# Optimization experiments

Hardware: AMD Instinct MI355X
Metric: run time of the kernel (lower is better)

The kernel has to match this reference:

```python
import jax, jax.numpy as jnp
import numpy as np

B, N, D, H = 8, 384, 256, 1024

def setup_inputs() -> dict:
    key = jax.random.key(0)
    ks = jax.random.split(key, 8)
    x = jax.random.normal(ks[0], (B, N, D), jnp.float32)
    adj = jnp.ones((B, N, N), jnp.float32)
    box_num = jax.random.randint(ks[1], (B, 1), 1, N + 1).astype(jnp.int64)
    box_num = box_num.at[0, 0].set(N)  # original code assumes max(box_num) == N
    fc1_w = jax.random.normal(ks[2], (H, D), jnp.float32) * (1.0 / np.sqrt(D))
    fc1_b = jnp.zeros((H,), jnp.float32)
    fc2_w = jax.random.normal(ks[3], (D, H), jnp.float32) * (1.0 / np.sqrt(H))
    fc2_b = jnp.zeros((D,), jnp.float32)
    learn_w = jax.random.uniform(ks[4], (D,), jnp.float32)  # uniform_(0,1) init
    return {"x": x, "adj": adj, "box_num": box_num,
            "fc1_w": fc1_w, "fc1_b": fc1_b, "fc2_w": fc2_w, "fc2_b": fc2_b,
            "learn_w": learn_w}

def reference(x, adj, box_num, fc1_w, fc1_b, fc2_w, fc2_b, learn_w):
    # mlp: fc2(relu(fc1(x)))  -> x_hat (B,N,D)
    x_hat = jnp.maximum(x @ fc1_w.T + fc1_b, 0.0) @ fc2_w.T + fc2_b
    # dynamic mask: -1 where either node i or j is padding, 0 otherwise
    valid = jnp.arange(N)[None, :] < box_num            # (B,N)
    pair_valid = valid[:, None, :] & valid[:, :, None]  # (B,N,N)
    mask = jnp.where(pair_valid, 0.0, -1.0)             # (B,N,N)
    # pairwise weighted L1 distance: einsum('bijd,d->bij', |x_i - x_j| + mask, w)
    # mask broadcasts over d, so its contribution is mask * sum(w) (same math,
    # avoids a second (B,N,N,D) materialization)
    absdiff = jnp.abs(x_hat[:, :, None, :] - x_hat[:, None, :, :])  # (B,N,N,D)
    dist = jnp.einsum('bijd,d->bij', absdiff, learn_w) + mask * jnp.sum(learn_w)
    out = jax.nn.leaky_relu(dist, negative_slope=0.01)
    out = out - jnp.max(out, axis=-1, keepdims=True)
    soft_adj = adj * jnp.exp(out)
    soft_adj = soft_adj / jnp.sum(soft_adj, axis=-1, keepdims=True) + 1e-10
    return soft_adj, x_hat
```

## Files before the change

### kernel.cpp

```cpp
#include <hip/hip_runtime.h>
#include <math.h>

#define B_ 8
#define N_ 384
#define D_ 256
#define H_ 1024

typedef __bf16 bh;
typedef __bf16 bf16x8 __attribute__((ext_vector_type(8)));
typedef __bf16 bf16x4 __attribute__((ext_vector_type(4)));
typedef float  f32x4  __attribute__((ext_vector_type(4)));
typedef _Float16 h2 __attribute__((ext_vector_type(2)));

#define LDB 72

#if __has_builtin(__builtin_amdgcn_fdot2)
#define FDOT2(a,b,c) __builtin_amdgcn_fdot2((a),(b),(c),false)
#else
#define FDOT2(a,b,c) ((c) + (float)(a).x*(float)(b).x + (float)(a).y*(float)(b).y)
#endif

__device__ inline h2 habs2(h2 x) {
    unsigned u = __builtin_bit_cast(unsigned, x) & 0x7fff7fffu;
    return __builtin_bit_cast(h2, u);
}

__device__ inline void split2(float v, bh& h, bh& l) {
    h = (bh)v;
    l = (bh)(v - (float)h);
}

__device__ inline int load_boxnum(const int* __restrict__ p, int b) {
    bool is64 = ((p[1] | p[3] | p[5] | p[7]) == 0);
    return is64 ? p[2 * b] : p[b];
}

__global__ __launch_bounds__(256) void split3_kernel(
        const float* __restrict__ s0, bh* __restrict__ h0, bh* __restrict__ l0, int n0,
        const float* __restrict__ s1, bh* __restrict__ h1, bh* __restrict__ l1, int n1,
        const float* __restrict__ s2, bh* __restrict__ h2_, bh* __restrict__ l2, int n2)
{
    const int total = n0 + n1 + n2;
    for (int qd = blockIdx.x * blockDim.x + threadIdx.x; qd < total; qd += gridDim.x * blockDim.x) {
        const float* s; bh* ph; bh* pl; int i;
        if (qd < n0)           { s = s0; ph = h0;  pl = l0; i = qd; }
        else if (qd < n0 + n1) { s = s1; ph = h1;  pl = l1; i = qd - n0; }
        else                   { s = s2; ph = h2_; pl = l2; i = qd - n0 - n1; }
        float4 v = *(const float4*)(s + 4 * (size_t)i);
        bf16x4 hv, lv; bh hh, ll;
        split2(v.x, hh, ll); hv[0] = hh; lv[0] = ll;
        split2(v.y, hh, ll); hv[1] = hh; lv[1] = ll;
        split2(v.z, hh, ll); hv[2] = hh; lv[2] = ll;
        split2(v.w, hh, ll); hv[3] = hh; lv[3] = ll;
        *(bf16x4*)(ph + 4 * (size_t)i) = hv;
        *(bf16x4*)(pl + 4 * (size_t)i) = lv;
    }
}

__global__ __launch_bounds__(256) void gemm1_kernel(
        const bh* __restrict__ Ah_, const bh* __restrict__ Al_,
        const bh* __restrict__ Wh_, const bh* __restrict__ Wl_,
        const float* __restrict__ bias,
        bh* __restrict__ Ch, bh* __restrict__ Cl)
{
    __shared__ __align__(16) bh AhS[64 * LDB], AlS[64 * LDB], WhS[64 * LDB], WlS[64 * LDB];
    const int tid = threadIdx.x;
    const int m0 = blockIdx.y * 64, n0 = blockIdx.x * 64;
    const int r = tid >> 2, kq = (tid & 3) * 16;
    const int lane = tid & 63, wv_ = tid >> 6;
    const int wm = (wv_ & 1) * 32, wn = (wv_ >> 1) * 32;
    const int l15 = lane & 15, q = lane >> 4;

    f32x4 acc[2][2] = {};
    for (int k0 = 0; k0 < D_; k0 += 64) {
        const bh* pah = Ah_ + (size_t)(m0 + r) * D_ + k0 + kq;
        const bh* pal = Al_ + (size_t)(m0 + r) * D_ + k0 + kq;
        const bh* pwh = Wh_ + (size_t)(n0 + r) * D_ + k0 + kq;
        const bh* pwl = Wl_ + (size_t)(n0 + r) * D_ + k0 + kq;
        bf16x8 ah0 = *(const bf16x8*)pah, ah1 = *(const bf16x8*)(pah + 8);
        bf16x8 al0 = *(const bf16x8*)pal, al1 = *(const bf16x8*)(pal + 8);
        bf16x8 wh0 = *(const bf16x8*)pwh, wh1 = *(const bf16x8*)(pwh + 8);
        bf16x8 wl0 = *(const bf16x8*)pwl, wl1 = *(const bf16x8*)(pwl + 8);
        __syncthreads();
        *(bf16x8*)&AhS[r * LDB + kq] = ah0;  *(bf16x8*)&AhS[r * LDB + kq + 8] = ah1;
        *(bf16x8*)&AlS[r * LDB + kq] = al0;  *(bf16x8*)&AlS[r * LDB + kq + 8] = al1;
        *(bf16x8*)&WhS[r * LDB + kq] = wh0;  *(bf16x8*)&WhS[r * LDB + kq + 8] = wh1;
        *(bf16x8*)&WlS[r * LDB + kq] = wl0;  *(bf16x8*)&WlS[r * LDB + kq + 8] = wl1;
        __syncthreads();
        #pragma unroll
        for (int ks = 0; ks < 2; ks++) {
            const int kb = ks * 32 + q * 8;
            bf16x8 fah[2], fal[2], fwh[2], fwl[2];
            #pragma unroll
            for (int mi = 0; mi < 2; mi++) {
                int row = wm + mi * 16 + l15;
                fah[mi] = *(const bf16x8*)&AhS[row * LDB + kb];
                fal[mi] = *(const bf16x8*)&AlS[row * LDB + kb];
            }
            #pragma unroll
            for (int ni = 0; ni < 2; ni++) {
                int row = wn + ni * 16 + l15;
                fwh[ni] = *(const bf16x8*)&WhS[row * LDB + kb];
                fwl[ni] = *(const bf16x8*)&WlS[row * LDB + kb];
            }
            #pragma unroll
            for (int mi = 0; mi < 2; mi++)
                #pragma unroll
                for (int ni = 0; ni < 2; ni++) {
                    acc[mi][ni] = __builtin_amdgcn_mfma_f32_16x16x32_bf16(fah[mi], fwh[ni], acc[mi][ni], 0, 0, 0);
                    acc[mi][ni] = __builtin_amdgcn_mfma_f32_16x16x32_bf16(fah[mi], fwl[ni], acc[mi][ni], 0, 0, 0);
                    acc[mi][ni] = __builtin_amdgcn_mfma_f32_16x16x32_bf16(fal[mi], fwh[ni], acc[mi][ni], 0, 0, 0);
                }
        }
    }
    #pragma unroll
    for (int ni = 0; ni < 2; ni++) {
        int col = n0 + wn + ni * 16 + l15;
        float bb = bias[col];
        #pragma unroll
        for (int mi = 0; mi < 2; mi++)
            #pragma unroll
            for (int reg = 0; reg < 4; reg++) {
                int row = m0 + wm + mi * 16 + q * 4 + reg;
                float v = fmaxf(acc[mi][ni][reg] + bb, 0.f);
                bh h, l; split2(v, h, l);
                size_t off = (size_t)row * H_ + col;
                Ch[off] = h; Cl[off] = l;
            }
    }
}

__global__ __launch_bounds__(256) void gemm2_kernel(
        const bh* __restrict__ Ah_, const bh* __restrict__ Al_,
        const bh* __restrict__ Wh_, const bh* __restrict__ Wl_,
        const float* __restrict__ bias,
        float* __restrict__ C, _Float16* __restrict__ C16)
{
    __shared__ __align__(16) bh AhS[64 * LDB], AlS[64 * LDB], WhS[32 * LDB], WlS[32 * LDB];
    const int tid = threadIdx.x;
    const int m0 = blockIdx.y * 64, n0 = blockIdx.x * 32;
    const int lane = tid & 63, wv_ = tid >> 6;
    const int wm = wv_ * 16;
    const int l15 = lane & 15, q = lane >> 4;
    const int r = tid >> 2, kq = (tid & 3) * 16;
    const int rw = tid >> 3, kw = (tid & 7) * 8;

    f32x4 acc[2] = {};
    for (int k0 = 0; k0 < H_; k0 += 64) {
        const bh* pah = Ah_ + (size_t)(m0 + r) * H_ + k0 + kq;
        const bh* pal = Al_ + (size_t)(m0 + r) * H_ + k0 + kq;
        const bh* pwh = Wh_ + (size_t)(n0 + rw) * H_ + k0 + kw;
        const bh* pwl = Wl_ + (size_t)(n0 + rw) * H_ + k0 + kw;
        bf16x8 ah0 = *(const bf16x8*)pah, ah1 = *(const bf16x8*)(pah + 8);
        bf16x8 al0 = *(const bf16x8*)pal, al1 = *(const bf16x8*)(pal + 8);
        bf16x8 wh0 = *(const bf16x8*)pwh;
        bf16x8 wl0 = *(const bf16x8*)pwl;
        __syncthreads();
        *(bf16x8*)&AhS[r * LDB + kq] = ah0;  *(bf16x8*)&AhS[r * LDB + kq + 8] = ah1;
        *(bf16x8*)&AlS[r * LDB + kq] = al0;  *(bf16x8*)&AlS[r * LDB + kq + 8] = al1;
        *(bf16x8*)&WhS[rw * LDB + kw] = wh0;
        *(bf16x8*)&WlS[rw * LDB + kw] = wl0;
        __syncthreads();
        #pragma unroll
        for (int ks = 0; ks < 2; ks++) {
            const int kb = ks * 32 + q * 8;
            const int arow = wm + l15;
            bf16x8 fah = *(const bf16x8*)&AhS[arow * LDB + kb];
            bf16x8 fal = *(const bf16x8*)&AlS[arow * LDB + kb];
            #pragma unroll
            for (int ni = 0; ni < 2; ni++) {
                int row = ni * 16 + l15;
                bf16x8 fwh = *(const bf16x8*)&WhS[row * LDB + kb];
                bf16x8 fwl = *(const bf16x8*)&WlS[row * LDB + kb];
                acc[ni] = __builtin_amdgcn_mfma_f32_16x16x32_bf16(fah, fwh, acc[ni], 0, 0, 0);
                acc[ni] = __builtin_amdgcn_mfma_f32_16x16x32_bf16(fah, fwl, acc[ni], 0, 0, 0);
                acc[ni] = __builtin_amdgcn_mfma_f32_16x16x32_bf16(fal, fwh, acc[ni], 0, 0, 0);
            }
        }
    }
    #pragma unroll
    for (int ni = 0; ni < 2; ni++) {
        int col = n0 + ni * 16 + l15;
        float bb = bias[col];
        #pragma unroll
        for (int reg = 0; reg < 4; reg++) {
            int row = m0 + wm + q * 4 + reg;
            float v = acc[ni][reg] + bb;
            C[(size_t)row * D_ + col] = v;
            C16[(size_t)row * D_ + col] = (_Float16)v;
        }
    }
}

#define DLX 132
__global__ __launch_bounds__(512) void dist_kernel(const _Float16* __restrict__ xh16,
                                                   const float* __restrict__ w,
                                                   const int* __restrict__ box_num,
                                                   float* __restrict__ dist) {
    __shared__ __align__(16) unsigned X[128 * DLX];
    __shared__ unsigned WkS[128];
    const int bidx = blockIdx.x;
    const int b = bidx / 21;
    int p = bidx % 21;
    int ti = 0;
    while (p >= 6 - ti) { p -= 6 - ti; ti++; }
    const int tj = ti + p;
    const int i0 = ti * 64, j0 = tj * 64;
    const int tid = threadIdx.x;
    const int lane = tid & 63;

    float sumw = w[lane] + w[lane + 64] + w[lane + 128] + w[lane + 192];
    #pragma unroll
    for (int off = 32; off > 0; off >>= 1) sumw += __shfl_xor(sumw, off);

    if (tid < 128) {
        float2 wp = *(const float2*)&w[2 * tid];
        h2 wv = {(_Float16)wp.x, (_Float16)wp.y};
        WkS[tid] = __builtin_bit_cast(unsigned, wv);
    }

    const int sr = tid >> 2, koff = (tid & 3) * 64;
    const int grow = (sr < 64) ? (i0 + sr) : (j0 + sr - 64);
    const _Float16* src = xh16 + ((size_t)b * N_ + grow) * D_ + koff;
    #pragma unroll
    for (int ld = 0; ld < 8; ld++) {
        uint4 v = *(const uint4*)(src + ld * 8);
        int k2 = (koff >> 1) + ld * 4;
        X[(k2 + 0) * DLX + sr] = v.x;
        X[(k2 + 1) * DLX + sr] = v.y;
        X[(k2 + 2) * DLX + sr] = v.z;
        X[(k2 + 3) * DLX + sr] = v.w;
    }
    __syncthreads();

    const int tx = tid & 31, ty = tid >> 5;
    float acc[4][2] = {};
    #pragma unroll 4
    for (int k2 = 0; k2 < 128; k2++) {
        uint4 av = *(const uint4*)&X[k2 * DLX + ty * 4];
        uint2 bv = *(const uint2*)&X[k2 * DLX + 64 + tx * 2];
        h2 wv = __builtin_bit_cast(h2, WkS[k2]);
        h2 ai[4] = {__builtin_bit_cast(h2, av.x), __builtin_bit_cast(h2, av.y),
                    __builtin_bit_cast(h2, av.z), __builtin_bit_cast(h2, av.w)};
        h2 bj[2] = {__builtin_bit_cast(h2, bv.x), __builtin_bit_cast(h2, bv.y)};
        #pragma unroll
        for (int ii = 0; ii < 4; ii++)
            #pragma unroll
            for (int jj = 0; jj < 2; jj++) {
                h2 d = habs2(ai[ii] - bj[jj]);
                acc[ii][jj] = FDOT2(d, wv, acc[ii][jj]);
            }
    }

    const int bn = load_boxnum(box_num, b);
    float m[4][2];
    #pragma unroll
    for (int ii = 0; ii < 4; ii++) {
        int i = i0 + ty * 4 + ii;
        bool vi = i < bn;
        #pragma unroll
        for (int jj = 0; jj < 2; jj++) {
            int j = j0 + tx * 2 + jj;
            float v = acc[ii][jj];
            if (!(vi && (j < bn))) v -= sumw;
            m[ii][jj] = v > 0.f ? v : 0.01f * v;
        }
    }
    #pragma unroll
    for (int ii = 0; ii < 4; ii++) {
        int i = i0 + ty * 4 + ii;
        float2 o = {m[ii][0], m[ii][1]};
        *(float2*)&dist[((size_t)b * N_ + i) * N_ + j0 + tx * 2] = o;
    }
    #pragma unroll
    for (int jj = 0; jj < 2; jj++) {
        int j = j0 + tx * 2 + jj;
        float4 o = {m[0][jj], m[1][jj], m[2][jj], m[3][jj]};
        *(float4*)&dist[((size_t)b * N_ + j) * N_ + i0 + ty * 4] = o;
    }
}

__global__ __launch_bounds__(256) void softmax_kernel(float* __restrict__ sa,
                                                      const float* __restrict__ adj) {
    const int row = blockIdx.x * 4 + (threadIdx.x >> 6);
    const int t = threadIdx.x & 63;
    float* prow = sa + (size_t)row * N_;
    const float* arow = adj + (size_t)row * N_;
    float v[6];
    float m = -1e30f;
    #pragma unroll
    for (int qq = 0; qq < 6; qq++) { v[qq] = prow[t + qq * 64]; m = fmaxf(m, v[qq]); }
    #pragma unroll
    for (int off = 32; off > 0; off >>= 1) m = fmaxf(m, __shfl_xor(m, off));
    float e[6];
    float s = 0.f;
    #pragma unroll
    for (int qq = 0; qq < 6; qq++) { e[qq] = arow[t + qq * 64] * expf(v[qq] - m); s += e[qq]; }
    #pragma unroll
    for (int off = 32; off > 0; off >>= 1) s += __shfl_xor(s, off);
    float inv = 1.0f / s;
    #pragma unroll
    for (int qq = 0; qq < 6; qq++) prow[t + qq * 64] = e[qq] * inv + 1e-10f;
}

extern "C" void kernel_launch(void* const* d_in, const int* in_sizes, int n_in,
                              void* d_out, int out_size, void* d_ws, size_t ws_size,
                              hipStream_t stream) {
    const float* x       = (const float*)d_in[0];
    const float* adj     = (const float*)d_in[1];
    const int*   box_num = (const int*)d_in[2];
    const float* fc1_w   = (const float*)d_in[3];
    const float* fc1_b   = (const float*)d_in[4];
    const float* fc2_w   = (const float*)d_in[5];
    const float* fc2_b   = (const float*)d_in[6];
    const float* learn_w = (const float*)d_in[7];

    float* soft_adj = (float*)d_out;
    float* xhat     = (float*)d_out + (size_t)B_ * N_ * N_;

    const int BN = B_ * N_;

    bh* w1h = (bh*)d_ws;
    bh* w1l = w1h + (size_t)H_ * D_;
    bh* w2h = w1l + (size_t)H_ * D_;
    bh* w2l = w2h + (size_t)D_ * H_;
    _Float16* xh16 = (_Float16*)(w2l + (size_t)D_ * H_);
    bh* cbase = (bh*)(xh16 + (size_t)BN * D_);
    const size_t fixed_bytes = (size_t)4 * H_ * D_ * 2 + (size_t)BN * D_ * 2;
    const size_t per_row = (size_t)(D_ * 2 + H_ * 2) * 2;

    long long avail = (long long)ws_size - (long long)fixed_bytes;
    long long mr = (avail > 0) ? (avail / (long long)per_row) : 0;
    if (mr > BN) mr = BN;
    mr &= ~63LL;
    if (mr < 64) mr = 64;
    const int max_rows = (int)mr;

    bool first = true;
    for (int m0 = 0; m0 < BN; m0 += max_rows) {
        int rows = BN - m0; if (rows > max_rows) rows = max_rows;
        bh* xh  = cbase;
        bh* xl  = xh + (size_t)max_rows * D_;
        bh* c1h = xl + (size_t)max_rows * D_;
        bh* c1l = c1h + (size_t)max_rows * H_;

        int n0q = rows * D_ / 4;
        int n1q = first ? (H_ * D_ / 4) : 0;
        int n2q = first ? (D_ * H_ / 4) : 0;
        split3_kernel<<<512, 256, 0, stream>>>(
            x + (size_t)m0 * D_, xh, xl, n0q,
            fc1_w, w1h, w1l, n1q,
            fc2_w, w2h, w2l, n2q);

        dim3 g1(H_ / 64, rows / 64);
        gemm1_kernel<<<g1, 256, 0, stream>>>(xh, xl, w1h, w1l, fc1_b, c1h, c1l);
        dim3 g2(D_ / 32, rows / 64);
        gemm2_kernel<<<g2, 256, 0, stream>>>(c1h, c1l, w2h, w2l, fc2_b,
                                             xhat + (size_t)m0 * D_, xh16 + (size_t)m0 * D_);
        first = false;
    }

    dist_kernel<<<B_ * 21, 512, 0, stream>>>(xh16, learn_w, box_num, soft_adj);

    softmax_kernel<<<BN / 4, 256, 0, stream>>>(soft_adj, adj);
}
```

Baseline: 123.9 us.

## Fuse bf16 hi/lo split into GEMM loads and widen gemm2 K tile

Drops the separate split3 kernel: gemm1 now loads fp32 x and fc1_w and splits them into bf16 hi/lo pairs in registers, and gemm2 does the same for fc2_w. This removes one launch and the write-then-reread of split copies in the workspace. gemm2 also doubles its K step to 128, with a wider LDS stride, so it needs fewer barriers per tile. The cost is redundant split arithmetic, since each weight tile is re-split by every block that reads it, plus more LDS per gemm2 block.

```diff
diff --git a/kernel.cpp b/kernel.cpp
--- a/kernel.cpp
+++ b/kernel.cpp
@@ -8,11 +8,11 @@
 
 typedef __bf16 bh;
 typedef __bf16 bf16x8 __attribute__((ext_vector_type(8)));
-typedef __bf16 bf16x4 __attribute__((ext_vector_type(4)));
 typedef float  f32x4  __attribute__((ext_vector_type(4)));
 typedef _Float16 h2 __attribute__((ext_vector_type(2)));
 
-#define LDB 72
+#define LDB  72
+#define LDK2 136
 
 #if __has_builtin(__builtin_amdgcn_fdot2)
 #define FDOT2(a,b,c) __builtin_amdgcn_fdot2((a),(b),(c),false)
@@ -30,36 +30,19 @@
     l = (bh)(v - (float)h);
 }
 
+__device__ inline void split8(const float* f, bf16x8& h8, bf16x8& l8) {
+    #pragma unroll
+    for (int i = 0; i < 8; i++) { bh h, l; split2(f[i], h, l); h8[i] = h; l8[i] = l; }
+}
+
 __device__ inline int load_boxnum(const int* __restrict__ p, int b) {
     bool is64 = ((p[1] | p[3] | p[5] | p[7]) == 0);
     return is64 ? p[2 * b] : p[b];
 }
 
-__global__ __launch_bounds__(256) void split3_kernel(
-        const float* __restrict__ s0, bh* __restrict__ h0, bh* __restrict__ l0, int n0,
-        const float* __restrict__ s1, bh* __restrict__ h1, bh* __restrict__ l1, int n1,
-        const float* __restrict__ s2, bh* __restrict__ h2_, bh* __restrict__ l2, int n2)
-{
-    const int total = n0 + n1 + n2;
-    for (int qd = blockIdx.x * blockDim.x + threadIdx.x; qd < total; qd += gridDim.x * blockDim.x) {
-        const float* s; bh* ph; bh* pl; int i;
-        if (qd < n0)           { s = s0; ph = h0;  pl = l0; i = qd; }
-        else if (qd < n0 + n1) { s = s1; ph = h1;  pl = l1; i = qd - n0; }
-        else                   { s = s2; ph = h2_; pl = l2; i = qd - n0 - n1; }
-        float4 v = *(const float4*)(s + 4 * (size_t)i);
-        bf16x4 hv, lv; bh hh, ll;
-        split2(v.x, hh, ll); hv[0] = hh; lv[0] = ll;
-        split2(v.y, hh, ll); hv[1] = hh; lv[1] = ll;
-        split2(v.z, hh, ll); hv[2] = hh; lv[2] = ll;
-        split2(v.w, hh, ll); hv[3] = hh; lv[3] = ll;
-        *(bf16x4*)(ph + 4 * (size_t)i) = hv;
-        *(bf16x4*)(pl + 4 * (size_t)i) = lv;
-    }
-}
-
 __global__ __launch_bounds__(256) void gemm1_kernel(
-        const bh* __restrict__ Ah_, const bh* __restrict__ Al_,
-        const bh* __restrict__ Wh_, const bh* __restrict__ Wl_,
+        const float* __restrict__ A,
+        const float* __restrict__ W,
         const float* __restrict__ bias,
         bh* __restrict__ Ch, bh* __restrict__ Cl)
 {
@@ -73,19 +56,22 @@
 
     f32x4 acc[2][2] = {};
     for (int k0 = 0; k0 < D_; k0 += 64) {
-        const bh* pah = Ah_ + (size_t)(m0 + r) * D_ + k0 + kq;
-        const bh* pal = Al_ + (size_t)(m0 + r) * D_ + k0 + kq;
-        const bh* pwh = Wh_ + (size_t)(n0 + r) * D_ + k0 + kq;
-        const bh* pwl = Wl_ + (size_t)(n0 + r) * D_ + k0 + kq;
-        bf16x8 ah0 = *(const bf16x8*)pah, ah1 = *(const bf16x8*)(pah + 8);
-        bf16x8 al0 = *(const bf16x8*)pal, al1 = *(const bf16x8*)(pal + 8);
-        bf16x8 wh0 = *(const bf16x8*)pwh, wh1 = *(const bf16x8*)(pwh + 8);
-        bf16x8 wl0 = *(const bf16x8*)pwl, wl1 = *(const bf16x8*)(pwl + 8);
+        const float* ap = A + (size_t)(m0 + r) * D_ + k0 + kq;
+        const float* wp = W + (size_t)(n0 + r) * D_ + k0 + kq;
+        float af[16], wf[16];
+        #pragma unroll
+        for (int u = 0; u < 4; u++) {
+            *(float4*)&af[4 * u] = *(const float4*)(ap + 4 * u);
+            *(float4*)&wf[4 * u] = *(const float4*)(wp + 4 * u);
+        }
+        bf16x8 ah0, ah1, al0, al1, wh0, wh1, wl0, wl1;
+        split8(af,     ah0, al0); split8(af + 8, ah1, al1);
+        split8(wf,     wh0, wl0); split8(wf + 8, wh1, wl1);
         __syncthreads();
-        *(bf16x8*)&AhS[r * LDB + kq] = ah0;  *(bf16x8*)&AhS[r * LDB + kq + 8] = ah1;
-        *(bf16x8*)&AlS[r * LDB + kq] = al0;  *(bf16x8*)&AlS[r * LDB + kq + 8] = al1;
-        *(bf16x8*)&WhS[r * LDB + kq] = wh0;  *(bf16x8*)&WhS[r * LDB + kq + 8] = wh1;
-        *(bf16x8*)&WlS[r * LDB + kq] = wl0;  *(bf16x8*)&WlS[r * LDB + kq + 8] = wl1;
+        *(bf16x8*)&AhS[r * LDB + kq]     = ah0;  *(bf16x8*)&AhS[r * LDB + kq + 8] = ah1;
+        *(bf16x8*)&AlS[r * LDB + kq]     = al0;  *(bf16x8*)&AlS[r * LDB + kq + 8] = al1;
+        *(bf16x8*)&WhS[r * LDB + kq]     = wh0;  *(bf16x8*)&WhS[r * LDB + kq + 8] = wh1;
+        *(bf16x8*)&WlS[r * LDB + kq]     = wl0;  *(bf16x8*)&WlS[r * LDB + kq + 8] = wl1;
         __syncthreads();
         #pragma unroll
         for (int ks = 0; ks < 2; ks++) {
@@ -132,46 +118,55 @@
 
 __global__ __launch_bounds__(256) void gemm2_kernel(
         const bh* __restrict__ Ah_, const bh* __restrict__ Al_,
-        const bh* __restrict__ Wh_, const bh* __restrict__ Wl_,
+        const float* __restrict__ W,
         const float* __restrict__ bias,
         float* __restrict__ C, _Float16* __restrict__ C16)
 {
-    __shared__ __align__(16) bh AhS[64 * LDB], AlS[64 * LDB], WhS[32 * LDB], WlS[32 * LDB];
+    __shared__ __align__(16) bh AhS[64 * LDK2], AlS[64 * LDK2], WhS[32 * LDK2], WlS[32 * LDK2];
     const int tid = threadIdx.x;
     const int m0 = blockIdx.y * 64, n0 = blockIdx.x * 32;
     const int lane = tid & 63, wv_ = tid >> 6;
     const int wm = wv_ * 16;
     const int l15 = lane & 15, q = lane >> 4;
-    const int r = tid >> 2, kq = (tid & 3) * 16;
-    const int rw = tid >> 3, kw = (tid & 7) * 8;
+    const int r = tid >> 2, kq = (tid & 3) * 32;
+    const int rw = tid >> 3, kw = (tid & 7) * 16;
 
     f32x4 acc[2] = {};
-    for (int k0 = 0; k0 < H_; k0 += 64) {
+    for (int k0 = 0; k0 < H_; k0 += 128) {
         const bh* pah = Ah_ + (size_t)(m0 + r) * H_ + k0 + kq;
         const bh* pal = Al_ + (size_t)(m0 + r) * H_ + k0 + kq;
-        const bh* pwh = Wh_ + (size_t)(n0 + rw) * H_ + k0 + kw;
-        const bh* pwl = Wl_ + (size_t)(n0 + rw) * H_ + k0 + kw;
-        bf16x8 ah0 = *(const bf16x8*)pah, ah1 = *(const bf16x8*)(pah + 8);
-        bf16x8 al0 = *(const bf16x8*)pal, al1 = *(const bf16x8*)(pal + 8);
-        bf16x8 wh0 = *(const bf16x8*)pwh;
-        bf16x8 wl0 = *(const bf16x8*)pwl;
+        bf16x8 va[4], vl[4];
+        #pragma unroll
+        for (int u = 0; u < 4; u++) {
+            va[u] = *(const bf16x8*)(pah + 8 * u);
+            vl[u] = *(const bf16x8*)(pal + 8 * u);
+        }
+        const float* wp = W + (size_t)(n0 + rw) * H_ + k0 + kw;
+        float wf[16];
+        #pragma unroll
+        for (int u = 0; u < 4; u++) *(float4*)&wf[4 * u] = *(const float4*)(wp + 4 * u);
+        bf16x8 wh0, wh1, wl0, wl1;
+        split8(wf,     wh0, wl0); split8(wf + 8, wh1, wl1);
         __syncthreads();
-        *(bf16x8*)&AhS[r * LDB + kq] = ah0;  *(bf16x8*)&AhS[r * LDB + kq + 8] = ah1;
-        *(bf16x8*)&AlS[r * LDB + kq] = al0;  *(bf16x8*)&AlS[r * LDB + kq + 8] = al1;
-        *(bf16x8*)&WhS[rw * LDB + kw] = wh0;
-        *(bf16x8*)&WlS[rw * LDB + kw] = wl0;
+        #pragma unroll
+        for (int u = 0; u < 4; u++) {
+            *(bf16x8*)&AhS[r * LDK2 + kq + 8 * u] = va[u];
+            *(bf16x8*)&AlS[r * LDK2 + kq + 8 * u] = vl[u];
+        }
+        *(bf16x8*)&WhS[rw * LDK2 + kw]     = wh0;  *(bf16x8*)&WhS[rw * LDK2 + kw + 8] = wh1;
+        *(bf16x8*)&WlS[rw * LDK2 + kw]     = wl0;  *(bf16x8*)&WlS[rw * LDK2 + kw + 8] = wl1;
         __syncthreads();
         #pragma unroll
-        for (int ks = 0; ks < 2; ks++) {
+        for (int ks = 0; ks < 4; ks++) {
             const int kb = ks * 32 + q * 8;
             const int arow = wm + l15;
-            bf16x8 fah = *(const bf16x8*)&AhS[arow * LDB + kb];
-            bf16x8 fal = *(const bf16x8*)&AlS[arow * LDB + kb];
+            bf16x8 fah = *(const bf16x8*)&AhS[arow * LDK2 + kb];
+            bf16x8 fal = *(const bf16x8*)&AlS[arow * LDK2 + kb];
             #pragma unroll
             for (int ni = 0; ni < 2; ni++) {
                 int row = ni * 16 + l15;
-                bf16x8 fwh = *(const bf16x8*)&WhS[row * LDB + kb];
-                bf16x8 fwl = *(const bf16x8*)&WlS[row * LDB + kb];
+                bf16x8 fwh = *(const bf16x8*)&WhS[row * LDK2 + kb];
+                bf16x8 fwl = *(const bf16x8*)&WlS[row * LDK2 + kb];
                 acc[ni] = __builtin_amdgcn_mfma_f32_16x16x32_bf16(fah, fwh, acc[ni], 0, 0, 0);
                 acc[ni] = __builtin_amdgcn_mfma_f32_16x16x32_bf16(fah, fwl, acc[ni], 0, 0, 0);
                 acc[ni] = __builtin_amdgcn_mfma_f32_16x16x32_bf16(fal, fwh, acc[ni], 0, 0, 0);
@@ -320,14 +315,10 @@
 
     const int BN = B_ * N_;
 
-    bh* w1h = (bh*)d_ws;
-    bh* w1l = w1h + (size_t)H_ * D_;
-    bh* w2h = w1l + (size_t)H_ * D_;
-    bh* w2l = w2h + (size_t)D_ * H_;
-    _Float16* xh16 = (_Float16*)(w2l + (size_t)D_ * H_);
+    _Float16* xh16 = (_Float16*)d_ws;
     bh* cbase = (bh*)(xh16 + (size_t)BN * D_);
-    const size_t fixed_bytes = (size_t)4 * H_ * D_ * 2 + (size_t)BN * D_ * 2;
-    const size_t per_row = (size_t)(D_ * 2 + H_ * 2) * 2;
+    const size_t fixed_bytes = (size_t)BN * D_ * 2;
+    const size_t per_row = (size_t)H_ * 2 * 2;
 
     long long avail = (long long)ws_size - (long long)fixed_bytes;
     long long mr = (avail > 0) ? (avail / (long long)per_row) : 0;
@@ -336,28 +327,16 @@
     if (mr < 64) mr = 64;
     const int max_rows = (int)mr;
 
-    bool first = true;
     for (int m0 = 0; m0 < BN; m0 += max_rows) {
         int rows = BN - m0; if (rows > max_rows) rows = max_rows;
-        bh* xh  = cbase;
-        bh* xl  = xh + (size_t)max_rows * D_;
-        bh* c1h = xl + (size_t)max_rows * D_;
+        bh* c1h = cbase;
         bh* c1l = c1h + (size_t)max_rows * H_;
 
-        int n0q = rows * D_ / 4;
-        int n1q = first ? (H_ * D_ / 4) : 0;
-        int n2q = first ? (D_ * H_ / 4) : 0;
-        split3_kernel<<<512, 256, 0, stream>>>(
-            x + (size_t)m0 * D_, xh, xl, n0q,
-            fc1_w, w1h, w1l, n1q,
-            fc2_w, w2h, w2l, n2q);
-
         dim3 g1(H_ / 64, rows / 64);
-        gemm1_kernel<<<g1, 256, 0, stream>>>(xh, xl, w1h, w1l, fc1_b, c1h, c1l);
+        gemm1_kernel<<<g1, 256, 0, stream>>>(x + (size_t)m0 * D_, fc1_w, fc1_b, c1h, c1l);
         dim3 g2(D_ / 32, rows / 64);
-        gemm2_kernel<<<g2, 256, 0, stream>>>(c1h, c1l, w2h, w2l, fc2_b,
+        gemm2_kernel<<<g2, 256, 0, stream>>>(c1h, c1l, fc2_w, fc2_b,
                                              xhat + (size_t)m0 * D_, xh16 + (size_t)m0 * D_);
-        first = false;
     }
 
     dist_kernel<<<B_ * 21, 512, 0, stream>>>(xh16, learn_w, box_num, soft_adj);
```

Measured after the change: 124.3 us (median of 2 runs). Within noise of the previous version (+0.4%).
